# Performance work log

Measured on AMD Instinct MI355X. Metric: run time of the kernel, lower is better.

## Reference

```python
import jax, jax.numpy as jnp
import numpy as np

NUM_HOPS = 2
GAMMA = 0.8


def setup_inputs() -> dict:
    key = jax.random.key(0)
    ks = jax.random.split(key, 17)
    B, L, V, E, M, Mt, R = 8, 128, 50257, 768, 400, 800, 40
    W = 0.02  # init scale for learned params
    return {
        'hidden_states': jax.random.normal(ks[0], (B, L, E), jnp.float32),
        'wte': jax.random.normal(ks[1], (V, E), jnp.float32) * W,
        'rel_emb': jax.random.normal(ks[2], (R, E), jnp.float32) * W,
        'W_s': jax.random.normal(ks[3], (NUM_HOPS, E, E), jnp.float32) * W,
        'W_n': jax.random.normal(ks[4], (NUM_HOPS, E, E), jnp.float32) * W,
        'W_r': jax.random.normal(ks[5], (NUM_HOPS, E, E), jnp.float32) * W,
        'W_triple': jax.random.normal(ks[6], (E, 3 * E), jnp.float32) * W,
        'gate_w': jax.random.normal(ks[7], (E,), jnp.float32) * W,
        'gate_b': jnp.zeros((), jnp.float32),
        'concept_ids': jax.random.randint(ks[8], (B, M), 0, V),
        'relation_ids': jax.random.randint(ks[9], (B, Mt), 0, R),
        'head_idx': jax.random.randint(ks[10], (B, Mt), 0, M),
        'tail_idx': jax.random.randint(ks[11], (B, Mt), 0, M),
        'triple_labels': jax.random.randint(ks[12], (B, Mt), 0, 2),
        'distances': jax.random.randint(ks[13], (B, M), 0, 3),
        'vocab_map': jax.random.randint(ks[14], (V,), 0, M),
        'map_mask': jax.random.randint(ks[15], (V,), 0, 2),
    }


def _triple_encoder(wte, rel_emb, W_s, W_n, W_r, concept_ids, relation_ids, head_idx, tail_idx):
    concept_repr = wte[concept_ids]      # B,M,E
    rel_repr = rel_emb[relation_ids]     # B,Mt,E

    def gcn(cr, rr, h, t):               # per-batch CompGCN, faithful to torch loop
        M = cr.shape[0]
        ch, rh = cr, rr
        for l in range(NUM_HOPS):
            upd = jnp.zeros_like(cr)
            upd = upd.at[t].add(cr[h] - rr)   # scatter_add(o) + scatter_add(-rel)
            upd = upd.at[h].add(cr[t] - rr)
            cnt = jnp.zeros((M,), cr.dtype).at[t].add(1.0).at[h].add(1.0)
            upd = cr @ W_s[l].T + (upd @ W_n[l].T) / jnp.clip(cnt, 1.0, None)[:, None]
            ch = jax.nn.relu(upd)
            rh = rr @ W_r[l].T
        return ch, rh

    node, relh = jax.vmap(gcn)(concept_repr, rel_repr, head_idx, tail_idx)
    E = node.shape[-1]
    hi = jnp.broadcast_to(head_idx[:, :, None], head_idx.shape + (E,))
    ti = jnp.broadcast_to(tail_idx[:, :, None], tail_idx.shape + (E,))
    hrep = jnp.take_along_axis(node, hi, axis=1)
    trep = jnp.take_along_axis(node, ti, axis=1)
    return jnp.concatenate([hrep, relh, trep], axis=-1)  # B,Mt,3E


def _multi_hop(triple_prob, distances, head, tail):
    B, L, Mt = triple_prob.shape
    M = distances.shape[1]
    dt = triple_prob.dtype
    init_mask = jnp.broadcast_to((distances == 0).astype(dt)[:, None, :], (B, L, M))
    decay = (0.8 ** distances.astype(dt))[:, None, :]
    head_b = jnp.broadcast_to(head[:, None, :], (B, L, Mt))

    def scatter_mean(vals, t):  # vals: L,Mt  t: Mt -> L,M
        s = jnp.zeros((L, M), vals.dtype).at[:, t].add(vals)
        c = jnp.zeros((M,), vals.dtype).at[t].add(1.0)
        return s / jnp.clip(c, 1.0, None)

    node_score = init_mask
    total = init_mask * (-100000.0)
    for _ in range(NUM_HOPS):
        ths = jnp.take_along_axis(node_score, head_b, axis=2)  # B,L,Mt
        upd = ths * GAMMA + triple_prob
        node_score = jax.vmap(scatter_mean)(upd, tail)          # B,L,M
        total = total + node_score * decay
    return total


def reference(hidden_states, wte, rel_emb, W_s, W_n, W_r, W_triple, gate_w, gate_b,
              concept_ids, relation_ids, head_idx, tail_idx, triple_labels,
              distances, vocab_map, map_mask):
    triple_repr = _triple_encoder(wte, rel_emb, W_s, W_n, W_r,
                                  concept_ids, relation_ids, head_idx, tail_idx)
    lm_probs = jax.nn.softmax(hidden_states @ wte.T, axis=-1)            # B,L,V
    tl = triple_repr @ W_triple.T                                        # B,Mt,E
    triple_prob = jax.nn.sigmoid(jnp.einsum('ble,bme->blm', hidden_states, tl))
    triple_prob = triple_prob * (triple_labels != -1)[:, None, :].astype(triple_prob.dtype)
    scores = _multi_hop(triple_prob, distances, head_idx, tail_idx)      # B,L,M
    concept_probs = jax.nn.softmax(scores, axis=-1)
    cpv = concept_probs[:, :, vocab_map]                                 # gather into vocab: B,L,V
    cpv = cpv * (map_mask != 0)[None, None, :].astype(cpv.dtype)
    gate = jax.nn.sigmoid(hidden_states @ gate_w + gate_b)[..., None]    # B,L,1
    probs = gate * cpv + (1.0 - gate) * lm_probs
    return probs
```

## Files before the change

kernel.cpp:

```cpp
#include <hip/hip_runtime.h>
#include <stdint.h>

#define HB 8
#define HL 128
#define HV 50257
#define HE 768
#define HM 400
#define HMT 800
#define HBL (HB*HL)
#define NTILES 393
#define ELD 50272
#define WTE_F4 ((long)HV*HE/4)

typedef __attribute__((ext_vector_type(4))) float f32x4;
typedef __attribute__((ext_vector_type(8))) short bf16x8;
typedef unsigned short u16;

struct u16x4 { u16 x, y, z, w; };

__device__ __forceinline__ u16 f2bf(float x){
  union { float f; uint32_t u; } v; v.f = x;
  uint32_t r = v.u + 0x7fffu + ((v.u >> 16) & 1u);
  return (u16)(r >> 16);
}
__device__ __forceinline__ float bf2f(u16 b){
  union { uint32_t u; float f; } v; v.u = ((uint32_t)b) << 16;
  return v.f;
}
__device__ __forceinline__ void glds(const u16* g, const u16* l){
  __builtin_amdgcn_global_load_lds(
      (const __attribute__((address_space(1))) void*)g,
      (__attribute__((address_space(3))) void*)l, 16, 0, 0);
}
__device__ __forceinline__ void cvt_slice(const float* __restrict__ src,
    u16* __restrict__ dst, long lo4, long n4, int relb, int nb){
  long i = lo4 + (long)relb*256 + threadIdx.x;
  const long end = lo4 + n4;
  const long stride = (long)nb*256;
  for (; i < end; i += stride) {
    float4 x = ((const float4*)src)[i];
    u16x4 y; y.x=f2bf(x.x); y.y=f2bf(x.y); y.z=f2bf(x.z); y.w=f2bf(x.w);
    ((u16x4*)dst)[i] = y;
  }
}

__global__ __launch_bounds__(256) void gcn_prep_k(const float* __restrict__ wte,
    const float* __restrict__ rel, const int* __restrict__ cids,
    const int* __restrict__ rids, const int* __restrict__ head,
    const int* __restrict__ tail, u16* __restrict__ An,
    const float* __restrict__ hs, const float* __restrict__ Wr1src,
    const float* __restrict__ Wt, const float* __restrict__ Ws1,
    const float* __restrict__ Wn1, const int* __restrict__ vmap,
    const int* __restrict__ mmask,
    u16* __restrict__ hid_b, u16* __restrict__ rel_b,
    u16* __restrict__ wr1, u16* __restrict__ wtT, u16* __restrict__ wcat,
    int* __restrict__ vmm, u16* __restrict__ wte_b){
  const int t = threadIdx.x;
  if (blockIdx.x >= 5840) {
    cvt_slice(wte, wte_b, 0, 2621440L, blockIdx.x - 5840, 2048);
    return;
  }
  if (blockIdx.x >= 384) {
    const int b = blockIdx.x - 384;
    if (b < 768) {
      int i = b*256 + t;
      float4 x = ((const float4*)hs)[i];
      u16x4 y; y.x=f2bf(x.x); y.y=f2bf(x.y); y.z=f2bf(x.z); y.w=f2bf(x.w);
      ((u16x4*)hid_b)[i] = y;
    } else if (b < 798) {
      int i = (b-768)*256 + t;
      float4 x = ((const float4*)rel)[i];
      u16x4 y; y.x=f2bf(x.x); y.y=f2bf(x.y); y.z=f2bf(x.z); y.w=f2bf(x.w);
      ((u16x4*)rel_b)[i] = y;
    } else if (b < 1374) {
      int i = (b-798)*256 + t;
      float4 x = ((const float4*)Wr1src)[i];
      u16x4 y; y.x=f2bf(x.x); y.y=f2bf(x.y); y.z=f2bf(x.z); y.w=f2bf(x.w);
      ((u16x4*)wr1)[i] = y;
    } else if (b < 3102) {
      int g = (b-1374)*256 + t;
      int f = g / 192, r = g - f*192, e0 = r*4;
      u16x4 y;
      y.x = f2bf(Wt[(long)(e0+0)*2304 + f]);
      y.y = f2bf(Wt[(long)(e0+1)*2304 + f]);
      y.z = f2bf(Wt[(long)(e0+2)*2304 + f]);
      y.w = f2bf(Wt[(long)(e0+3)*2304 + f]);
      *(u16x4*)&wtT[(long)f*HE + e0] = y;
    } else if (b < 5406) {
      int i = (b-3102)*256 + t;
      int e = i / HE, k = i - e*HE;
      wcat[(long)e*(2*HE) + k]      = f2bf(Ws1[i]);
      wcat[(long)e*(2*HE) + HE + k] = f2bf(Wn1[i]);
    } else {
      int base = (b-5406)*1024 + t*4;
      #pragma unroll
      for (int i = 0; i < 4; ++i) {
        int c = base + i;
        if (c < HV) vmm[c] = mmask[c] ? vmap[c] : -1;
      }
    }
    return;
  }
  const int ch = blockIdx.x % 48;
  const int b  = blockIdx.x / 48;
  const int e0 = ch * 16;
  __shared__ float cw[HM][17];
  __shared__ float upd[HM][17];
  __shared__ float relc[40][17];
  __shared__ float cnt[HM];
  const int tid = t;

  for (int idx = tid; idx < HM*16; idx += 256) {
    int m = idx >> 4, e = idx & 15;
    cw[m][e] = wte[(long)cids[b*HM+m]*HE + e0 + e];
    upd[m][e] = 0.f;
  }
  for (int idx = tid; idx < 40*16; idx += 256) {
    int r = idx >> 4, e = idx & 15;
    relc[r][e] = rel[r*HE + e0 + e];
  }
  for (int m = tid; m < HM; m += 256) cnt[m] = 0.f;
  __syncthreads();

  for (int j = tid; j < HMT; j += 256) {
    int h = head[b*HMT+j], tt = tail[b*HMT+j], r = rids[b*HMT+j];
    atomicAdd(&cnt[tt], 1.f);
    atomicAdd(&cnt[h], 1.f);
    #pragma unroll
    for (int e = 0; e < 16; ++e) {
      float rv = relc[r][e];
      atomicAdd(&upd[tt][e], cw[h][e] - rv);
      atomicAdd(&upd[h][e], cw[tt][e] - rv);
    }
  }
  __syncthreads();

  for (int idx = tid; idx < HM*16; idx += 256) {
    int m = idx >> 4, e = idx & 15;
    float ic = 1.f / fmaxf(cnt[m], 1.f);
    u16* dst = An + ((long)b*HM + m) * (2*HE);
    dst[e0 + e]      = f2bf(cw[m][e]);
    dst[HE + e0 + e] = f2bf(upd[m][e] * ic);
  }
}

template<int ACT, int OUTBF16, int DBUF>
__device__ __forceinline__ void gemm_core(
    const u16* __restrict__ Ab, const u16* __restrict__ Bb,
    void* __restrict__ Cout,
    int Mdim, int Ndim, int Kdim, int lda, int ldb, int ldc,
    int mtile, int ntile, u16* AsmB, u16* BsmB)
{
  const int m0 = mtile * 128;
  const int n0 = ntile * 128;
  const int tid = threadIdx.x;
  const int lane = tid & 63;
  const int wid = tid >> 6;
  const int wr = wid >> 1, wc = wid & 1;
  const int srw = lane >> 3;
  const int sl  = lane & 7;

  f32x4 acc[4][4] = {};

  auto stage = [&](int buf, int k0) {
    u16* As = AsmB + buf*8192;
    u16* Bs = BsmB + buf*8192;
    #pragma unroll
    for (int i = 0; i < 4; ++i) {
      const int c = i*4 + wid;
      const int row = c*8 + srw;
      const int koff = k0 + ((sl ^ srw) * 8);
      int ra = m0 + row; if (ra > Mdim-1) ra = Mdim-1;
      glds(Ab + (long)ra * lda + koff, &As[c*512]);
      int rn = n0 + row; if (rn > Ndim-1) rn = Ndim-1;
      glds(Bb + (long)rn * ldb + koff, &Bs[c*512]);
    }
  };
  auto compute = [&](int buf) {
    const u16* As = AsmB + buf*8192;
    const u16* Bs = BsmB + buf*8192;
    #pragma unroll
    for (int kk = 0; kk < 2; ++kk) {
      bf16x8 af[4], bfr[4];
      #pragma unroll
      for (int mi = 0; mi < 4; ++mi) {
        const int R = wr*64 + mi*16 + (lane & 15);
        af[mi] = *(const bf16x8*)&As[R*64 + (((kk*4 + (lane>>4)) ^ (R & 7)) * 8)];
      }
      #pragma unroll
      for (int ni = 0; ni < 4; ++ni) {
        const int R = wc*64 + ni*16 + (lane & 15);
        bfr[ni] = *(const bf16x8*)&Bs[R*64 + (((kk*4 + (lane>>4)) ^ (R & 7)) * 8)];
      }
      #pragma unroll
      for (int mi = 0; mi < 4; ++mi)
        #pragma unroll
        for (int ni = 0; ni < 4; ++ni)
          acc[mi][ni] = __builtin_amdgcn_mfma_f32_16x16x32_bf16(af[mi], bfr[ni], acc[mi][ni], 0, 0, 0);
    }
  };

  const int NT = Kdim >> 6;
  if (DBUF) {
    stage(0, 0);
    asm volatile("s_waitcnt vmcnt(0)" ::: "memory");
    __builtin_amdgcn_s_barrier();
    int cur = 0;
    for (int t = 0; t < NT; ++t) {
      if (t + 1 < NT) {
        stage(cur ^ 1, (t + 1) << 6);
        asm volatile("s_waitcnt vmcnt(8)" ::: "memory");
      } else {
        asm volatile("s_waitcnt vmcnt(0)" ::: "memory");
      }
      __builtin_amdgcn_s_barrier();
      compute(cur);
      __builtin_amdgcn_s_barrier();
      cur ^= 1;
    }
  } else {
    for (int t = 0; t < NT; ++t) {
      stage(0, t << 6);
      __syncthreads();
      compute(0);
      __syncthreads();
    }
  }

  const int cr0 = m0 + wr*64 + ((lane >> 4) * 4);
  const int cc0 = n0 + wc*64 + (lane & 15);
  #pragma unroll
  for (int mi = 0; mi < 4; ++mi) {
    #pragma unroll
    for (int ni = 0; ni < 4; ++ni) {
      const int col = cc0 + ni*16;
      if (col < Ndim) {
        #pragma unroll
        for (int r = 0; r < 4; ++r) {
          const int rowi = cr0 + mi*16 + r;
          if (rowi < Mdim) {
            float v = acc[mi][ni][r];
            if (ACT == 1) v = fmaxf(v, 0.f);
            if (OUTBF16) ((u16*)Cout)[(long)rowi*ldc + col] = f2bf(v);
            else        ((float*)Cout)[(long)rowi*ldc + col] = v;
          }
        }
      }
    }
  }
}

template<int EXPBF>
__global__ __launch_bounds__(256) void gemm_big(
    const u16* __restrict__ A, const u16* __restrict__ Bm,
    void* __restrict__ Cout, float* __restrict__ rowpart,
    int Mdim, int Ndim, int Kdim, int lda, int ldb, int ldc)
{
  __shared__ alignas(16) u16 Asm[3*4096];
  __shared__ alignas(16) u16 Bsm[3*4096];
  const int wg = (blockIdx.x & 7) * NTILES + (blockIdx.x >> 3);
  const int m0 = (wg & 7) * 128;
  const int n0 = (wg >> 3) * 128;
  const int ntile = wg >> 3;
  const int tid = threadIdx.x;
  const int lane = tid & 63;
  const int wid = tid >> 6;
  const int wr = wid >> 1, wc = wid & 1;
  const int srow = lane >> 2;
  const int sl = lane & 3;

  f32x4 acc[4][4] = {};

  auto stage = [&](int buf, int k0) {
    u16* As = Asm + buf*4096;
    u16* Bs = Bsm + buf*4096;
    const int koff = k0 + ((sl ^ ((srow >> 1) & 3)) * 8);
    #pragma unroll
    for (int i = 0; i < 2; ++i) {
      const int c = i*4 + wid;
      const int row = c*16 + srow;
      int ra = m0 + row; if (ra > Mdim-1) ra = Mdim-1;
      glds(A + (long)ra*lda + koff, &As[c*512]);
      int rn = n0 + row; if (rn > Ndim-1) rn = Ndim-1;
      glds(Bm + (long)rn*ldb + koff, &Bs[c*512]);
    }
  };
  auto compute = [&](int buf) {
    const u16* As = Asm + buf*4096;
    const u16* Bs = Bsm + buf*4096;
    bf16x8 af[4], bfr[4];
    #pragma unroll
    for (int mi = 0; mi < 4; ++mi) {
      const int R = wr*64 + mi*16 + (lane & 15);
      af[mi] = *(const bf16x8*)&As[R*32 + (((lane>>4) ^ ((R >> 1) & 3)) * 8)];
    }
    #pragma unroll
    for (int ni = 0; ni < 4; ++ni) {
      const int R = wc*64 + ni*16 + (lane & 15);
      bfr[ni] = *(const bf16x8*)&Bs[R*32 + (((lane>>4) ^ ((R >> 1) & 3)) * 8)];
    }
    #pragma unroll
    for (int ni = 0; ni < 4; ++ni)
      #pragma unroll
      for (int mi = 0; mi < 4; ++mi)
        acc[ni][mi] = __builtin_amdgcn_mfma_f32_16x16x32_bf16(bfr[ni], af[mi], acc[ni][mi], 0, 0, 0);
  };

  const int NT = Kdim >> 5;
  stage(0, 0);
  stage(1, 32);
  int cur = 0;
  for (int t = 0; t < NT; ++t) {
    if (t + 2 < NT) {
      int sb = cur + 2; if (sb >= 3) sb -= 3;
      stage(sb, (t + 2) << 5);
      asm volatile("s_waitcnt vmcnt(8)" ::: "memory");
    } else if (t + 1 < NT) {
      asm volatile("s_waitcnt vmcnt(4)" ::: "memory");
    } else {
      asm volatile("s_waitcnt vmcnt(0)" ::: "memory");
    }
    __builtin_amdgcn_s_barrier();
    compute(cur);
    __builtin_amdgcn_s_barrier();
    cur = (cur == 2) ? 0 : cur + 1;
  }

  const int f = lane & 15;
  float* rs = (float*)Asm;
  #pragma unroll
  for (int mi = 0; mi < 4; ++mi) {
    const int rowi = m0 + wr*64 + mi*16 + f;
    float s = 0.f;
    #pragma unroll
    for (int ni = 0; ni < 4; ++ni) {
      const int cb = n0 + wc*64 + ni*16 + (lane >> 4)*4;
      f32x4 a = acc[ni][mi];
      float e0 = __expf(a[0]), e1 = __expf(a[1]);
      float e2 = __expf(a[2]), e3 = __expf(a[3]);
      if (cb + 3 < Ndim) {
        s += e0 + e1 + e2 + e3;
        if (EXPBF) {
          ushort4 y; y.x=f2bf(e0); y.y=f2bf(e1); y.z=f2bf(e2); y.w=f2bf(e3);
          *(ushort4*)&((u16*)Cout)[(long)rowi*ldc + cb] = y;
        } else {
          float* dst = &((float*)Cout)[(long)rowi*ldc + cb];
          dst[0]=e0; dst[1]=e1; dst[2]=e2; dst[3]=e3;
        }
      } else {
        float ev[4] = {e0, e1, e2, e3};
        for (int i = 0; i < 4; ++i) {
          if (cb + i < Ndim) {
            s += ev[i];
            if (EXPBF) ((u16*)Cout)[(long)rowi*ldc + cb + i] = f2bf(ev[i]);
            else      ((float*)Cout)[(long)rowi*ldc + cb + i] = ev[i];
          }
        }
      }
    }
    s += __shfl_xor(s, 16);
    s += __shfl_xor(s, 32);
    if ((lane >> 4) == 0) rs[wc*128 + wr*64 + mi*16 + f] = s;
  }
  __syncthreads();
  if (tid < 128)
    rowpart[(long)(m0 + tid) * NTILES + ntile] = rs[tid] + rs[128 + tid];
}

__global__ __launch_bounds__(256) void gemm_multi0(
    const u16* __restrict__ anode, const u16* __restrict__ wcat,
    u16* __restrict__ nodeb, const u16* __restrict__ rel_b,
    const u16* __restrict__ wr1, u16* __restrict__ relWr,
    const u16* __restrict__ hid_b, const u16* __restrict__ wtT,
    u16* __restrict__ hw, const float* __restrict__ wte,
    u16* __restrict__ wte_b)
{
  if (blockIdx.x >= 342) {
    cvt_slice(wte, wte_b, 2621440L, 4194304L, blockIdx.x - 342, 4096);
    return;
  }
  __shared__ alignas(16) u16 Asm[2*8192];
  __shared__ alignas(16) u16 Bsm[2*8192];
  const int q = blockIdx.x;
  if (q < 192) {
    const int z = q / 24, r = q - z*24;
    gemm_core<1,1,1>(anode + (long)z*HM*2*HE, wcat, nodeb + (long)z*HM*HE,
        HM, HE, 2*HE, 2*HE, 2*HE, HE, r & 3, r >> 2, Asm, Bsm);
  } else if (q < 198) {
    gemm_core<0,1,1>(rel_b, wr1, relWr,
        40, HE, HE, HE, HE, HE, 0, q - 192, Asm, Bsm);
  } else {
    const int u = q - 198;
    gemm_core<0,1,1>(hid_b, wtT, hw,
        HBL, 3*HE, HE, HE, HE, 3*HE, u & 7, u >> 3, Asm, Bsm);
  }
}

__global__ __launch_bounds__(256) void gemm_multi1(
    const u16* __restrict__ hw, const u16* __restrict__ nodeb,
    const u16* __restrict__ relWr, float* __restrict__ scores,
    const float* __restrict__ wte, u16* __restrict__ wte_b)
{
  if (blockIdx.x >= 72) {
    cvt_slice(wte, wte_b, 6815744L, 1572864L, blockIdx.x - 72, 1536);
    return;
  }
  __shared__ alignas(16) u16 Asm[2*8192];
  __shared__ alignas(16) u16 Bsm[2*8192];
  const int q = blockIdx.x;
  if (q < 32) {
    const int z = q >> 2;
    gemm_core<0,0,1>(hw + (long)z*HL*(3*HE), nodeb + (long)z*HM*HE,
        scores + (long)z*HL*840,
        HL, HM, HE, 3*HE, HE, 840, 0, q & 3, Asm, Bsm);
  } else if (q < 64) {
    const int z = (q - 32) >> 2;
    gemm_core<0,0,1>(hw + (long)z*HL*(3*HE) + 2*HE, nodeb + (long)z*HM*HE,
        scores + (long)z*HL*840 + HM,
        HL, HM, HE, 3*HE, HE, 840, 0, (q - 32) & 3, Asm, Bsm);
  } else {
    gemm_core<0,0,1>(hw + HE, relWr, scores + 2*HM,
        HBL, 40, HE, 3*HE, HE, 840, q - 64, 0, Asm, Bsm);
  }
}

__global__ __launch_bounds__(256) void multihop_k(const float* __restrict__ scores,
    const float* __restrict__ hs, const float* __restrict__ gw,
    const float* __restrict__ gb,
    const int* __restrict__ head, const int* __restrict__ tail,
    const int* __restrict__ rids, const int* __restrict__ labels,
    const int* __restrict__ dist, float* __restrict__ gatev,
    float* __restrict__ cprob, const float* __restrict__ wte,
    u16* __restrict__ wte_b){
  if (blockIdx.x >= HBL) {
    cvt_slice(wte, wte_b, 8388608L, WTE_F4 - 8388608L, blockIdx.x - HBL, 1280);
    return;
  }
  const int bl = blockIdx.x;
  const int b = bl >> 7;
  const int tid = threadIdx.x;
  const int lane = tid & 63, wid = tid >> 6;
  __shared__ float srow[840];
  __shared__ float tp[HMT];
  __shared__ float ns[HM], sacc[HM], tot[HM], invc[HM], dec[HM];
  __shared__ float red[16];
  __shared__ float gred[4];
  const int* hb = head + b*HMT;
  const int* tb = tail + b*HMT;
  const int* rb = rids + b*HMT;
  const int* lb = labels + b*HMT;
  const float* sr = scores + (long)bl * 840;

  float gs = 0.f;
  for (int e = tid; e < HE; e += 256) gs += hs[(long)bl*HE + e] * gw[e];
  for (int o = 32; o; o >>= 1) gs += __shfl_down(gs, o);
  if (lane == 0) gred[wid] = gs;

  for (int i = tid; i < 840; i += 256) srow[i] = sr[i];
  for (int m = tid; m < HM; m += 256) {
    int d = dist[b*HM + m];
    float im = (d == 0) ? 1.f : 0.f;
    ns[m] = im; tot[m] = im * -100000.f;
    dec[m] = (d == 0) ? 1.f : ((d == 1) ? 0.8f : 0.64f);
    sacc[m] = 0.f; invc[m] = 0.f;
  }
  __syncthreads();
  if (tid == 0)
    gatev[bl] = 1.f / (1.f + __expf(-(gred[0]+gred[1]+gred[2]+gred[3] + gb[0])));
  for (int j = tid; j < HMT; j += 256) {
    atomicAdd(&invc[tb[j]], 1.f);
    float x = srow[hb[j]] + srow[HM + tb[j]] + srow[2*HM + rb[j]];
    tp[j] = (lb[j] == -1) ? 0.f : 1.f / (1.f + __expf(-x));
  }
  __syncthreads();
  for (int m = tid; m < HM; m += 256) invc[m] = 1.f / fmaxf(invc[m], 1.f);
  __syncthreads();

  for (int hop = 0; hop < 2; ++hop) {
    for (int j = tid; j < HMT; j += 256) {
      float u = ns[hb[j]] * 0.8f + tp[j];
      atomicAdd(&sacc[tb[j]], u);
    }
    __syncthreads();
    for (int m = tid; m < HM; m += 256) {
      float v = sacc[m] * invc[m];
      ns[m] = v; tot[m] += v * dec[m]; sacc[m] = 0.f;
    }
    __syncthreads();
  }

  float lmx = -3.4e38f;
  for (int m = tid; m < HM; m += 256) lmx = fmaxf(lmx, tot[m]);
  for (int o = 32; o; o >>= 1) lmx = fmaxf(lmx, __shfl_down(lmx, o));
  if (lane == 0) red[wid] = lmx;
  __syncthreads();
  float gmx = fmaxf(fmaxf(red[0], red[1]), fmaxf(red[2], red[3]));
  float ls = 0.f;
  for (int m = tid; m < HM; m += 256) ls += __expf(tot[m] - gmx);
  for (int o = 32; o; o >>= 1) ls += __shfl_down(ls, o);
  if (lane == 0) red[8 + wid] = ls;
  __syncthreads();
  float inv = 1.f / (red[8] + red[9] + red[10] + red[11]);
  float* outrow = cprob + (long)bl * HM;
  for (int m = tid; m < HM; m += 256) outrow[m] = __expf(tot[m] - gmx) * inv;
}

template<int EXPBF>
__global__ __launch_bounds__(256) void finalize_k(const void* __restrict__ expl,
    const float* __restrict__ rowpart, const float* __restrict__ gatev,
    const float* __restrict__ cprob, const int* __restrict__ vmm,
    float* __restrict__ out){
  const int r = blockIdx.x / 13;
  const int ch = blockIdx.x - r*13;
  const int tid = threadIdx.x;
  __shared__ float red[4];
  __shared__ float cpl[HM];
  float s = 0.f;
  for (int t = tid; t < NTILES; t += 256) s += rowpart[r*NTILES + t];
  for (int o = 32; o; o >>= 1) s += __shfl_down(s, o);
  if ((tid & 63) == 0) red[tid >> 6] = s;
  const float g = gatev[r];
  for (int m = tid; m < HM; m += 256) cpl[m] = g * cprob[r*HM + m];
  __syncthreads();
  const float scale = (1.f - g) / (red[0] + red[1] + red[2] + red[3]);
  const u16* erb = (const u16*)expl + (long)r * ELD;
  const float* erf = (const float*)expl + (long)r * HV;
  float* orow = out + (long)r * HV;
  #pragma unroll
  for (int it = 0; it < 2; ++it) {
    const int c = ch*4096 + it*2048 + tid*8;
    if (c + 8 <= HV) {
      float e[8];
      if (EXPBF) {
        bf16x8 v = *(const bf16x8*)&erb[c];
        #pragma unroll
        for (int i = 0; i < 8; ++i) e[i] = bf2f((u16)v[i]);
      } else {
        float4 a = *(const float4*)&erf[c];
        float4 b2 = *(const float4*)&erf[c+4];
        e[0]=a.x; e[1]=a.y; e[2]=a.z; e[3]=a.w;
        e[4]=b2.x; e[5]=b2.y; e[6]=b2.z; e[7]=b2.w;
      }
      int4 v0 = *(const int4*)&vmm[c];
      int4 v1 = *(const int4*)&vmm[c+4];
      const int ix[8] = {v0.x, v0.y, v0.z, v0.w, v1.x, v1.y, v1.z, v1.w};
      float o8[8];
      #pragma unroll
      for (int i = 0; i < 8; ++i)
        o8[i] = (ix[i] >= 0 ? cpl[ix[i]] : 0.f) + scale * e[i];
      *(float4*)&orow[c]   = make_float4(o8[0], o8[1], o8[2], o8[3]);
      *(float4*)&orow[c+4] = make_float4(o8[4], o8[5], o8[6], o8[7]);
    } else if (c < HV) {
      for (int i = 0; i < 8 && c + i < HV; ++i) {
        float e = EXPBF ? bf2f(((const u16*)expl)[(long)r*ELD + c + i]) : erf[c+i];
        int ix = vmm[c+i];
        orow[c+i] = (ix >= 0 ? cpl[ix] : 0.f) + scale * e;
      }
    }
  }
}

extern "C" void kernel_launch(void* const* d_in, const int* in_sizes, int n_in,
                              void* d_out, int out_size, void* d_ws, size_t ws_size,
                              hipStream_t stream)
{
  const float* hs   = (const float*)d_in[0];
  const float* wte  = (const float*)d_in[1];
  const float* rel  = (const float*)d_in[2];
  const float* Ws   = (const float*)d_in[3];
  const float* Wn   = (const float*)d_in[4];
  const float* Wr   = (const float*)d_in[5];
  const float* Wt   = (const float*)d_in[6];
  const float* gw   = (const float*)d_in[7];
  const float* gb   = (const float*)d_in[8];
  const int* cids   = (const int*)d_in[9];
  const int* rids   = (const int*)d_in[10];
  const int* head   = (const int*)d_in[11];
  const int* tail   = (const int*)d_in[12];
  const int* labels = (const int*)d_in[13];
  const int* dist   = (const int*)d_in[14];
  const int* vmap   = (const int*)d_in[15];
  const int* mmask  = (const int*)d_in[16];
  float* out = (float*)d_out;

  char* ws = (char*)d_ws;
  size_t o = 0;
  auto alloc = [&](size_t bytes) -> char* {
    char* p = ws + o; o = (o + bytes + 255) & ~(size_t)255; return p;
  };
  u16* wte_b     = (u16*)alloc((size_t)HV*HE*2);
  u16* hid_b     = (u16*)alloc((size_t)HBL*HE*2);
  float* cprob   = (float*)alloc((size_t)HBL*HM*4);
  float* rowpart = (float*)alloc((size_t)HBL*NTILES*4);
  float* gatev   = (float*)alloc(HBL*4);
  int* vmm       = (int*)alloc((size_t)HV*4);
  float* scores  = (float*)alloc((size_t)HBL*840*4);

  const bool bigws = ws_size >= (size_t)196*1024*1024;
  u16* expl = (u16*)(ws + o);
  u16* wcat  = (u16*)alloc((size_t)HE*2*HE*2);
  u16* wr1   = (u16*)alloc((size_t)HE*HE*2);
  u16* wtT   = (u16*)alloc((size_t)3*HE*HE*2);
  u16* rel_b = (u16*)alloc((size_t)40*HE*2);
  u16* anode = (u16*)alloc((size_t)HB*HM*2*HE*2);
  u16* nodeb = (u16*)alloc((size_t)HB*HM*HE*2);
  u16* relWr = (u16*)alloc((size_t)40*HE*2);
  u16* hw    = (u16*)alloc((size_t)HBL*3*HE*2);
  (void)in_sizes; (void)n_in; (void)out_size;

  gcn_prep_k<<<5840 + 2048, 256, 0, stream>>>(wte, rel, cids, rids, head,
      tail, anode, hs, Wr + (size_t)HE*HE, Wt, Ws + (size_t)HE*HE,
      Wn + (size_t)HE*HE, vmap, mmask,
      hid_b, rel_b, wr1, wtT, wcat, vmm, wte_b);

  gemm_multi0<<<342 + 4096, 256, 0, stream>>>(anode, wcat, nodeb, rel_b, wr1,
      relWr, hid_b, wtT, hw, wte, wte_b);
  gemm_multi1<<<72 + 1536, 256, 0, stream>>>(hw, nodeb, relWr, scores,
      wte, wte_b);

  multihop_k<<<HBL + 1280, 256, 0, stream>>>(scores, hs, gw, gb, head, tail,
      rids, labels, dist, gatev, cprob, wte, wte_b);

  if (bigws) {
    gemm_big<1><<<3144, 256, 0, stream>>>(hid_b, wte_b, expl, rowpart,
        HBL, HV, HE, HE, HE, ELD);
    finalize_k<1><<<HBL*13, 256, 0, stream>>>(expl, rowpart, gatev, cprob,
        vmm, out);
  } else {
    gemm_big<0><<<3144, 256, 0, stream>>>(hid_b, wte_b, out, rowpart,
        HBL, HV, HE, HE, HE, HV);
    finalize_k<0><<<HBL*13, 256, 0, stream>>>(out, rowpart, gatev, cprob,
        vmm, out);
  }
}
```

Measured before the change: 384.0 us.

## Enlarge LM-head GEMM tiles to 256x256 with 512-thread blocks and split MFMA phases

The vocab-projection GEMM now uses 256x256 output tiles computed by 8 waves (512 threads) instead of 128x128 tiles with 4 waves. Each wave holds a 128x64 accumulator block, split into two MFMA phases wrapped in s_setprio. The XCD-aware workgroup remapping is redone for the new 788-block grid, and the row-partial-sum buffer shrinks to 197 column tiles. The larger tiles aim to raise arithmetic intensity and cut redundant global/LDS loads. In exchange the kernel uses more registers and LDS, and only 788 workgroups cover the GPU's CUs, which may reduce occupancy and leave a tail imbalance.

```diff
diff --git a/kernel.cpp b/kernel.cpp
--- a/kernel.cpp
+++ b/kernel.cpp
@@ -8,7 +8,7 @@
 #define HM 400
 #define HMT 800
 #define HBL (HB*HL)
-#define NTILES 393
+#define NT2 197
 #define ELD 50272
 #define WTE_F4 ((long)HV*HE/4)
 
@@ -251,59 +251,45 @@
 }
 
 template<int EXPBF>
-__global__ __launch_bounds__(256) void gemm_big(
+__global__ __launch_bounds__(512) void gemm_big(
     const u16* __restrict__ A, const u16* __restrict__ Bm,
     void* __restrict__ Cout, float* __restrict__ rowpart,
     int Mdim, int Ndim, int Kdim, int lda, int ldb, int ldc)
 {
-  __shared__ alignas(16) u16 Asm[3*4096];
-  __shared__ alignas(16) u16 Bsm[3*4096];
-  const int wg = (blockIdx.x & 7) * NTILES + (blockIdx.x >> 3);
-  const int m0 = (wg & 7) * 128;
-  const int n0 = (wg >> 3) * 128;
-  const int ntile = wg >> 3;
+  __shared__ alignas(16) u16 Asm[3*8192];
+  __shared__ alignas(16) u16 Bsm[3*8192];
+  const int orig = blockIdx.x;
+  const int xcd = orig & 7;
+  const int qq = 788/8, rr = 788%8;
+  const int wg = (xcd < rr ? xcd*(qq+1) : rr*(qq+1) + (xcd-rr)*qq) + (orig>>3);
+  const int mtile = wg & 3;
+  const int ntile = wg >> 2;
+  const int m0 = mtile << 8;
+  const int n0 = ntile << 8;
   const int tid = threadIdx.x;
   const int lane = tid & 63;
   const int wid = tid >> 6;
-  const int wr = wid >> 1, wc = wid & 1;
-  const int srow = lane >> 2;
-  const int sl = lane & 3;
-
-  f32x4 acc[4][4] = {};
+  const int wr = wid >> 2;
+  const int wc = wid & 3;
+  const int f = lane & 15;
+  const int g4 = lane >> 4;
+
+  f32x4 acc[8][4] = {};
 
   auto stage = [&](int buf, int k0) {
-    u16* As = Asm + buf*4096;
-    u16* Bs = Bsm + buf*4096;
-    const int koff = k0 + ((sl ^ ((srow >> 1) & 3)) * 8);
+    u16* As = Asm + buf*8192;
+    u16* Bs = Bsm + buf*8192;
     #pragma unroll
     for (int i = 0; i < 2; ++i) {
-      const int c = i*4 + wid;
-      const int row = c*16 + srow;
+      const int gbase = wid*128 + i*64;
+      const int idx = gbase + lane;
+      const int row = idx >> 2, g = idx & 3;
+      const int koff = k0 + ((g ^ ((row >> 1) & 3)) * 8);
       int ra = m0 + row; if (ra > Mdim-1) ra = Mdim-1;
-      glds(A + (long)ra*lda + koff, &As[c*512]);
+      glds(A + (long)ra*lda + koff, &As[gbase*8]);
       int rn = n0 + row; if (rn > Ndim-1) rn = Ndim-1;
-      glds(Bm + (long)rn*ldb + koff, &Bs[c*512]);
-    }
-  };
-  auto compute = [&](int buf) {
-    const u16* As = Asm + buf*4096;
-    const u16* Bs = Bsm + buf*4096;
-    bf16x8 af[4], bfr[4];
-    #pragma unroll
-    for (int mi = 0; mi < 4; ++mi) {
-      const int R = wr*64 + mi*16 + (lane & 15);
-      af[mi] = *(const bf16x8*)&As[R*32 + (((lane>>4) ^ ((R >> 1) & 3)) * 8)];
-    }
-    #pragma unroll
-    for (int ni = 0; ni < 4; ++ni) {
-      const int R = wc*64 + ni*16 + (lane & 15);
-      bfr[ni] = *(const bf16x8*)&Bs[R*32 + (((lane>>4) ^ ((R >> 1) & 3)) * 8)];
-    }
-    #pragma unroll
-    for (int ni = 0; ni < 4; ++ni)
-      #pragma unroll
-      for (int mi = 0; mi < 4; ++mi)
-        acc[ni][mi] = __builtin_amdgcn_mfma_f32_16x16x32_bf16(bfr[ni], af[mi], acc[ni][mi], 0, 0, 0);
+      glds(Bm + (long)rn*ldb + koff, &Bs[gbase*8]);
+    }
   };
 
   const int NT = Kdim >> 5;
@@ -321,21 +307,52 @@
       asm volatile("s_waitcnt vmcnt(0)" ::: "memory");
     }
     __builtin_amdgcn_s_barrier();
-    compute(cur);
+    const u16* As = Asm + cur*8192;
+    const u16* Bs = Bsm + cur*8192;
+    bf16x8 af[4], bfr[4];
+    #pragma unroll
+    for (int ni = 0; ni < 4; ++ni) {
+      const int R = wc*64 + ni*16 + f;
+      bfr[ni] = *(const bf16x8*)&Bs[R*32 + ((g4 ^ ((R >> 1) & 3)) * 8)];
+    }
+    #pragma unroll
+    for (int k = 0; k < 4; ++k) {
+      const int R = wr*128 + k*16 + f;
+      af[k] = *(const bf16x8*)&As[R*32 + ((g4 ^ ((R >> 1) & 3)) * 8)];
+    }
+    __builtin_amdgcn_s_setprio(1);
+    #pragma unroll
+    for (int k = 0; k < 4; ++k)
+      #pragma unroll
+      for (int ni = 0; ni < 4; ++ni)
+        acc[k][ni] = __builtin_amdgcn_mfma_f32_16x16x32_bf16(bfr[ni], af[k], acc[k][ni], 0, 0, 0);
+    __builtin_amdgcn_s_setprio(0);
+    __builtin_amdgcn_s_barrier();
+    #pragma unroll
+    for (int k = 0; k < 4; ++k) {
+      const int R = wr*128 + (4 + k)*16 + f;
+      af[k] = *(const bf16x8*)&As[R*32 + ((g4 ^ ((R >> 1) & 3)) * 8)];
+    }
+    __builtin_amdgcn_s_setprio(1);
+    #pragma unroll
+    for (int k = 0; k < 4; ++k)
+      #pragma unroll
+      for (int ni = 0; ni < 4; ++ni)
+        acc[4 + k][ni] = __builtin_amdgcn_mfma_f32_16x16x32_bf16(bfr[ni], af[k], acc[4 + k][ni], 0, 0, 0);
+    __builtin_amdgcn_s_setprio(0);
     __builtin_amdgcn_s_barrier();
     cur = (cur == 2) ? 0 : cur + 1;
   }
 
-  const int f = lane & 15;
   float* rs = (float*)Asm;
   #pragma unroll
-  for (int mi = 0; mi < 4; ++mi) {
-    const int rowi = m0 + wr*64 + mi*16 + f;
+  for (int mi = 0; mi < 8; ++mi) {
+    const int rowi = m0 + wr*128 + mi*16 + f;
     float s = 0.f;
     #pragma unroll
     for (int ni = 0; ni < 4; ++ni) {
-      const int cb = n0 + wc*64 + ni*16 + (lane >> 4)*4;
-      f32x4 a = acc[ni][mi];
+      const int cb = n0 + wc*64 + ni*16 + g4*4;
+      f32x4 a = acc[mi][ni];
       float e0 = __expf(a[0]), e1 = __expf(a[1]);
       float e2 = __expf(a[2]), e3 = __expf(a[3]);
       if (cb + 3 < Ndim) {
@@ -360,11 +377,12 @@
     }
     s += __shfl_xor(s, 16);
     s += __shfl_xor(s, 32);
-    if ((lane >> 4) == 0) rs[wc*128 + wr*64 + mi*16 + f] = s;
-  }
-  __syncthreads();
-  if (tid < 128)
-    rowpart[(long)(m0 + tid) * NTILES + ntile] = rs[tid] + rs[128 + tid];
+    if (g4 == 0) rs[(wr*128 + mi*16 + f)*4 + wc] = s;
+  }
+  __syncthreads();
+  if (tid < 256)
+    rowpart[(long)(m0 + tid)*NT2 + ntile] =
+        rs[tid*4] + rs[tid*4+1] + rs[tid*4+2] + rs[tid*4+3];
 }
 
 __global__ __launch_bounds__(256) void gemm_multi0(
@@ -516,7 +534,7 @@
   __shared__ float red[4];
   __shared__ float cpl[HM];
   float s = 0.f;
-  for (int t = tid; t < NTILES; t += 256) s += rowpart[r*NTILES + t];
+  for (int t = tid; t < NT2; t += 256) s += rowpart[r*NT2 + t];
   for (int o = 32; o; o >>= 1) s += __shfl_down(s, o);
   if ((tid & 63) == 0) red[tid >> 6] = s;
   const float g = gatev[r];
@@ -591,7 +609,7 @@
   u16* wte_b     = (u16*)alloc((size_t)HV*HE*2);
   u16* hid_b     = (u16*)alloc((size_t)HBL*HE*2);
   float* cprob   = (float*)alloc((size_t)HBL*HM*4);
-  float* rowpart = (float*)alloc((size_t)HBL*NTILES*4);
+  float* rowpart = (float*)alloc((size_t)HBL*NT2*4);
   float* gatev   = (float*)alloc(HBL*4);
   int* vmm       = (int*)alloc((size_t)HV*4);
   float* scores  = (float*)alloc((size_t)HBL*840*4);
@@ -622,12 +640,12 @@
       rids, labels, dist, gatev, cprob, wte, wte_b);
 
   if (bigws) {
-    gemm_big<1><<<3144, 256, 0, stream>>>(hid_b, wte_b, expl, rowpart,
+    gemm_big<1><<<788, 512, 0, stream>>>(hid_b, wte_b, expl, rowpart,
         HBL, HV, HE, HE, HE, ELD);
     finalize_k<1><<<HBL*13, 256, 0, stream>>>(expl, rowpart, gatev, cprob,
         vmm, out);
   } else {
-    gemm_big<0><<<3144, 256, 0, stream>>>(hid_b, wte_b, out, rowpart,
+    gemm_big<0><<<788, 512, 0, stream>>>(hid_b, wte_b, out, rowpart,
         HBL, HV, HE, HE, HE, HV);
     finalize_k<0><<<HBL*13, 256, 0, stream>>>(out, rowpart, gatev, cprob,
         vmm, out);
```

Measured after the change: 403.7 us. 1.05x slower.
